# Performance work log

Hardware: AMD Instinct MI355X
Metric: run time of the kernel (lower is better)

The kernel has to match this reference:

```python
import jax, jax.numpy as jnp
import numpy as np

TWO_THIRDS = 2.0 / 3.0
SEVENTEEN_SIXTHS = 17.0 / 6.0


def _grid():
    # torch: cat(-flip(logspace(-2,2,100)**2), [0], logspace(-2,2,100)**2) -> 201 points
    gp = jnp.logspace(-2.0, 2.0, 100, dtype=jnp.float32) ** 2
    return jnp.concatenate([-gp[::-1], jnp.zeros((1,), jnp.float32), gp])


def _trapz_w(x):
    # trapezoidal quadrature weights so that trapz(f, x) == sum(f * w)
    dx = jnp.diff(x)
    w = jnp.zeros_like(x)
    return w.at[:-1].add(0.5 * dx).at[1:].add(0.5 * dx)


def setup_inputs() -> dict:
    key = jax.random.key(0)
    k1k, kyk, kzk = jax.random.split(key, 3)
    k1 = jnp.sort(jax.random.uniform(k1k, (512,), jnp.float32, 0.01, 1.0))  # positive wavenumbers
    dy = jax.random.uniform(kyk, (64,), jnp.float32, 0.0, 50.0)  # spanwise separations [m]
    dz = jax.random.uniform(kzk, (64,), jnp.float32, 0.0, 50.0)  # vertical separations [m]
    return {
        "k1_input": k1,
        "Delta_y": dy,
        "Delta_z": dz,
        "logLengthScale": jnp.float32(np.log(0.7 * 42.0)),
        "logTimeScale": jnp.float32(np.log(3.9)),
        "logMagnitude": jnp.float32(0.0),
    }


def reference(k1_input, Delta_y, Delta_z, logLengthScale, logTimeScale, logMagnitude):
    L = jnp.exp(logLengthScale)
    T = jnpp = jnp.exp(logTimeScale)
    M = jnp.exp(logMagnitude)
    k2g = _grid()  # [201]
    k3g = _grid()  # [201]
    # broadcasted meshgrid (never materialize a 4D stacked k tensor)
    k1 = k1_input[:, None, None]   # [Nk1,1,1]
    k2 = k2g[None, :, None]        # [1,201,1]
    k3 = k3g[None, None, :]        # [1,1,201]
    kk = k1 * k1 + k2 * k2 + k3 * k3
    # EddyLifetime 'TwoThird': beta = T * (L*|k|)^{-2/3}
    beta = T * (L * jnp.sqrt(kk)) ** (-TWO_THIRDS)
    k30 = k3 + beta * k1
    kk0 = k1 * k1 + k2 * k2 + k30 * k30
    k0L = L * jnp.sqrt(kk0)
    # von Karman energy spectrum at distorted wavevector
    E0 = M * k0L ** 4 / (1.0 + k0L * k0L) ** SEVENTEEN_SIXTHS
    # RDT spectral tensor, 11-component (module uses Phi[0] for Phi11, Phi33 and Phi13)
    s = k1 * k1 + k2 * k2
    C1 = beta * k1 * k1 * (kk0 - 2.0 * k30 * k30 + beta * k1 * k30) / (kk * s)
    C2 = k2 * kk0 / s ** 1.5 * jnp.arctan2(beta * k1 * jnp.sqrt(s), kk0 - k30 * k1 * beta)
    zeta1 = C1 - (k2 / k1) * C2
    Phi11 = E0 / (4.0 * jnp.pi * kk0 * kk0) * (
        kk0 - k1 * k1 - 2.0 * k1 * k30 * zeta1 + s * zeta1 * zeta1
    )  # [Nk1,201,201]
    # double trapezoid over (k2,k3) as weighted sums
    w2 = _trapz_w(k2g)
    w3 = _trapz_w(k3g)
    F1 = jnp.einsum('aij,i,j->a', Phi11, w2, w3)  # = F3
    den = jnp.sqrt(F1 * F1)
    # exp(i(k2*dy + k3*dz)) is separable -> factor the nested loop into two einsums
    Pw = (Phi11 * w2[None, :, None] * w3[None, None, :]).astype(jnp.complex64)
    E3 = jnp.exp(1j * k3g[:, None] * Delta_z[None, :])  # [201,Nz]
    E2 = jnp.exp(1j * k2g[:, None] * Delta_y[None, :])  # [201,Ny]
    A = jnp.einsum('aij,jz->aiz', Pw, E3)   # [Nk1,201,Nz]
    I = jnp.einsum('aiz,iy->ayz', A, E2)    # [Nk1,Ny,Nz]
    return jnp.real(I) / den[:, None, None]
```

## Files before the change

kernel.cpp:

```cpp
#include <hip/hip_runtime.h>
#include <math.h>

#define BLOCK 256
#define LOG2_10 3.3219280948873623f
#define PI_F 3.14159265358979f
#define INV2PI 0.15915494309189535f
#define PW_SCALE 256.0f

#define SP 128
#define SA 128
#define ST 64

typedef _Float16 half8 __attribute__((ext_vector_type(8)));
typedef _Float16 half4 __attribute__((ext_vector_type(4)));
typedef _Float16 half2v __attribute__((ext_vector_type(2)));
typedef float f32x4 __attribute__((ext_vector_type(4)));

__device__ __forceinline__ float fast_cos(float x_rev) {
    return __builtin_amdgcn_cosf(__builtin_amdgcn_fractf(x_rev));
}

__device__ __forceinline__ float atan2_pos(float y, float x) {
    float ax = __builtin_fabsf(x);
    float mn = fminf(ax, y), mx = fmaxf(ax, y);
    float a = mn * __builtin_amdgcn_rcpf(mx);
    float t = a * a;
    float p = fmaf(fmaf(fmaf(fmaf(fmaf(-0.0117212f, t, 0.05265332f), t,
              -0.11643287f), t, 0.19354346f), t, -0.33262347f), t, 0.99997726f);
    p *= a;
    p = (y > ax) ? (1.57079632679f - p) : p;
    p = (x < 0.0f) ? (3.14159265359f - p) : p;
    return p;
}

__global__ __launch_bounds__(BLOCK, 2)
void spectral_kernel(const float* __restrict__ k1_in,
                     const float* __restrict__ dy_in,
                     const float* __restrict__ dz_in,
                     const float* __restrict__ plogL,
                     const float* __restrict__ plogT,
                     const float* __restrict__ plogM,
                     float* __restrict__ out)
{
    __shared__ __attribute__((aligned(16))) _Float16 s_phiT[32 * SP];
    __shared__ __attribute__((aligned(16))) _Float16 s_B3T[64 * SP];
    __shared__ __attribute__((aligned(16))) _Float16 s_A2[64 * SA];
    __shared__ __attribute__((aligned(16))) _Float16 s_TcT[64 * ST];
    __shared__ float  s_grid[204];
    __shared__ float2 s_gw[204];
    __shared__ float  s_dy[64], s_dz[64];
    __shared__ float  s_red[8];

    const int t    = threadIdx.x;
    const int a    = blockIdx.x;
    const int lane = t & 63;
    const int w    = t >> 6;
    const int n16  = lane & 15;
    const int quad = lane >> 4;

    const float L  = expf(plogL[0]);
    const float Tt = expf(plogT[0]);
    const float M  = expf(plogM[0]);
    const float L2 = L * L;
    const float k1   = k1_in[a];
    const float k1sq = k1 * k1;
    const float rk1  = __builtin_amdgcn_rcpf(k1);
    const float cM0  = (M * 0.25f / PI_F) * PW_SCALE;

    if (t < 204) {
        int tt = min(t, 200);
        float v;
        if (tt < 100)       v = -exp2f(LOG2_10 * (-4.0f + 8.0f * (float)(99 - tt) * (1.0f/99.0f)));
        else if (tt == 100) v = 0.0f;
        else                v =  exp2f(LOG2_10 * (-4.0f + 8.0f * (float)(tt - 101) * (1.0f/99.0f)));
        s_grid[t] = v;
    }
    if (t < 64) { s_dy[t] = dy_in[t]; s_dz[t] = dz_in[t]; }
    __syncthreads();

    if (t < 204) {
        float wv = 0.0f;
        if (t == 0)          wv = 0.5f * (s_grid[1] - s_grid[0]);
        else if (t < 200)    wv = 0.5f * (s_grid[t+1] - s_grid[t-1]);
        else if (t == 200)   wv = 0.5f * (s_grid[200] - s_grid[199]);
        s_gw[t] = make_float2(s_grid[t], wv);
    }
    {
        const int jjp = lane;
        const int jj0 = 2 * jjp, jj1 = jj0 + 1;
        const float g0 = s_grid[min(100 + jj0, 203)];
        const float g1 = s_grid[min(100 + jj1, 203)];
        const int jjg  = jjp >> 2;
        for (int m = 0; m < 16; ++m) {
            int z = w + 4 * m;
            float dzr = s_dz[z] * INV2PI;
            float c0 = (jj0 <= 100) ? fast_cos(g0 * dzr) : 0.0f;
            float c1 = (jj1 <= 100) ? fast_cos(g1 * dzr) : 0.0f;
            half2v pr; pr.x = (_Float16)c0; pr.y = (_Float16)c1;
            *(half2v*)&s_B3T[z * SP + ((jjg ^ (z & 7)) << 3) + (jj0 & 7)] = pr;
        }
    }
    {
        float dyr = s_dy[lane] * INV2PI;
        for (int k = 0; k < 16; ++k) {
            int iip = w + 4 * k;
            int i0 = 2 * iip, i1 = i0 + 1;
            float c0 = (i0 <= 100) ? fast_cos(s_grid[min(100 + i0, 203)] * dyr) : 0.0f;
            float c1 = (i1 <= 100) ? fast_cos(s_grid[min(100 + i1, 203)] * dyr) : 0.0f;
            half2v pr; pr.x = (_Float16)c0; pr.y = (_Float16)c1;
            int off = lane * SA + (((iip >> 2) ^ (lane & 7)) << 3) + ((iip & 3) << 1);
            *(half2v*)&s_A2[off] = pr;
        }
    }
    {
        half8 zz = {};
        *(half8*)&s_phiT[t * 8] = zz;
        *(half8*)&s_phiT[(t + 256) * 8] = zz;
    }
    __syncthreads();

    float f1 = 0.0f;
    f32x4 acc2[4];
    #pragma unroll
    for (int i = 0; i < 4; ++i) acc2[i] = (f32x4){0.f, 0.f, 0.f, 0.f};

    const int il = t >> 3;
    const int jb = t & 7;

    for (int c = 0; c < 4; ++c) {
        if (c < 3) {
            const int ii = c * 32 + il;
            const float k2  = s_gw[100 + ii].x;
            const float w2m = s_gw[100 + ii].y * ((ii == 0) ? 1.0f : 2.0f);
            const float cM  = cM0 * w2m;
            const float s   = k1sq + k2 * k2;
            const float rs  = __builtin_amdgcn_rsqf(s);
            const float sqs = s * rs;
            const float s15inv = rs * rs * rs;
            const float k2ok1  = k2 * rk1;

            #pragma unroll 2
            for (int k = 0; k < 13; ++k) {
                const int jj = jb + (k << 3);
                const bool act = (jj <= 100);
                const float2 gwv = s_gw[100 + (act ? jj : 0)];
                const float g = gwv.x, w3 = gwv.y;
                const float kk   = fmaf(g, g, s);
                const float beta = Tt * __builtin_amdgcn_exp2f((-1.0f/3.0f) * __builtin_amdgcn_logf(L2 * kk));
                const float bk1  = beta * k1;
                const float rkks = __builtin_amdgcn_rcpf(kk * s);
                const float bkk1 = bk1 * k1;
                float k30a = bk1 - g,        k30b = bk1 + g;
                float k3sa = k30a * k30a,    k3sb = k30b * k30b;
                float kk0a = s + k3sa,       kk0b = s + k3sb;
                float ua   = L2 * kk0a,      ub   = L2 * kk0b;
                float e0a  = ua * ua * __builtin_amdgcn_exp2f((-17.0f/6.0f) * __builtin_amdgcn_logf(1.0f + ua));
                float e0b  = ub * ub * __builtin_amdgcn_exp2f((-17.0f/6.0f) * __builtin_amdgcn_logf(1.0f + ub));
                float C1a  = bkk1 * (s - k3sa + bk1 * k30a) * rkks;
                float C1b  = bkk1 * (s - k3sb + bk1 * k30b) * rkks;
                float tha  = atan2_pos(bk1 * sqs, kk0a - k30a * bk1);
                float thb  = atan2_pos(bk1 * sqs, kk0b - k30b * bk1);
                float za   = C1a - k2ok1 * (k2 * kk0a * s15inv * tha);
                float zb   = C1b - k2ok1 * (k2 * kk0b * s15inv * thb);
                float rka  = __builtin_amdgcn_rcpf(kk0a);
                float rkb  = __builtin_amdgcn_rcpf(kk0b);
                float qqa  = fmaf(fmaf(s, za, -2.0f * k1 * k30a), za, kk0a - k1sq);
                float qqb  = fmaf(fmaf(s, zb, -2.0f * k1 * k30b), zb, kk0b - k1sq);
                float pws  = fmaf(e0a * qqa, rka * rka, e0b * qqb * rkb * rkb);
                float scale = (jj == 0) ? 0.5f : 1.0f;
                float val = act ? (pws * cM * w3 * scale) : 0.0f;
                f1 += val;
                s_phiT[il * SP + (((jj >> 3) ^ (il & 7)) << 3) + (jj & 7)] = (_Float16)val;
            }
        } else {
            for (int idx = t; idx < 432; idx += 256) {
                half8 zz = {};
                *(half8*)&s_phiT[5 * SP + idx * 8] = zz;
            }
            #pragma unroll
            for (int m = 0; m < 2; ++m) {
                const int widx = t + 256 * m;
                if (widx < 505) {
                    const int il3 = widx / 101;
                    const int jj  = widx - il3 * 101;
                    const int ii  = 96 + il3;
                    const float k2  = s_gw[100 + ii].x;
                    const float cM  = cM0 * (s_gw[100 + ii].y * 2.0f);
                    const float s   = k1sq + k2 * k2;
                    const float rs  = __builtin_amdgcn_rsqf(s);
                    const float sqs = s * rs;
                    const float s15inv = rs * rs * rs;
                    const float k2ok1  = k2 * rk1;
                    const float2 gwv = s_gw[100 + jj];
                    const float g = gwv.x, w3 = gwv.y;
                    const float kk   = fmaf(g, g, s);
                    const float beta = Tt * __builtin_amdgcn_exp2f((-1.0f/3.0f) * __builtin_amdgcn_logf(L2 * kk));
                    const float bk1  = beta * k1;
                    const float rkks = __builtin_amdgcn_rcpf(kk * s);
                    const float bkk1 = bk1 * k1;
                    float k30a = bk1 - g,        k30b = bk1 + g;
                    float k3sa = k30a * k30a,    k3sb = k30b * k30b;
                    float kk0a = s + k3sa,       kk0b = s + k3sb;
                    float ua   = L2 * kk0a,      ub   = L2 * kk0b;
                    float e0a  = ua * ua * __builtin_amdgcn_exp2f((-17.0f/6.0f) * __builtin_amdgcn_logf(1.0f + ua));
                    float e0b  = ub * ub * __builtin_amdgcn_exp2f((-17.0f/6.0f) * __builtin_amdgcn_logf(1.0f + ub));
                    float C1a  = bkk1 * (s - k3sa + bk1 * k30a) * rkks;
                    float C1b  = bkk1 * (s - k3sb + bk1 * k30b) * rkks;
                    float tha  = atan2_pos(bk1 * sqs, kk0a - k30a * bk1);
                    float thb  = atan2_pos(bk1 * sqs, kk0b - k30b * bk1);
                    float za   = C1a - k2ok1 * (k2 * kk0a * s15inv * tha);
                    float zb   = C1b - k2ok1 * (k2 * kk0b * s15inv * thb);
                    float rka  = __builtin_amdgcn_rcpf(kk0a);
                    float rkb  = __builtin_amdgcn_rcpf(kk0b);
                    float qqa  = fmaf(fmaf(s, za, -2.0f * k1 * k30a), za, kk0a - k1sq);
                    float qqb  = fmaf(fmaf(s, zb, -2.0f * k1 * k30b), zb, kk0b - k1sq);
                    float pws  = fmaf(e0a * qqa, rka * rka, e0b * qqb * rkb * rkb);
                    float scale = (jj == 0) ? 0.5f : 1.0f;
                    float val = pws * cM * w3 * scale;
                    f1 += val;
                    s_phiT[il3 * SP + (((jj >> 3) ^ (il3 & 7)) << 3) + (jj & 7)] = (_Float16)val;
                }
            }
        }
        __syncthreads();

        {
            const int mt  = w & 1;
            const int nt0 = (w >> 1) << 1;
            f32x4 acc1a = {0.f,0.f,0.f,0.f}, acc1b = {0.f,0.f,0.f,0.f};
            const int arow  = mt * 16 + n16;
            const int brow0 = nt0 * 16 + n16;
            const int brow1 = brow0 + 16;
            #pragma unroll
            for (int ks = 0; ks < 4; ++ks) {
                int kg = ks * 4 + quad;
                half8 af  = *(const half8*)&s_phiT[arow  * SP + ((kg ^ (arow  & 7)) << 3)];
                half8 bf0 = *(const half8*)&s_B3T [brow0 * SP + ((kg ^ (brow0 & 7)) << 3)];
                half8 bf1 = *(const half8*)&s_B3T [brow1 * SP + ((kg ^ (brow1 & 7)) << 3)];
                acc1a = __builtin_amdgcn_mfma_f32_16x16x32_f16(af, bf0, acc1a, 0, 0, 0);
                acc1b = __builtin_amdgcn_mfma_f32_16x16x32_f16(af, bf1, acc1b, 0, 0, 0);
            }
            const int ii0 = mt * 16 + quad * 4;
            const int g   = ii0 >> 3;
            const int wi  = ii0 & 7;
            {
                int z = brow0;
                half4 hv; hv.x=(_Float16)acc1a.x; hv.y=(_Float16)acc1a.y;
                hv.z=(_Float16)acc1a.z; hv.w=(_Float16)acc1a.w;
                *(half4*)&s_TcT[z * ST + ((g ^ (z & 7)) << 3) + wi] = hv;
            }
            {
                int z = brow1;
                half4 hv; hv.x=(_Float16)acc1b.x; hv.y=(_Float16)acc1b.y;
                hv.z=(_Float16)acc1b.z; hv.w=(_Float16)acc1b.w;
                *(half4*)&s_TcT[z * ST + ((g ^ (z & 7)) << 3) + wi] = hv;
            }
        }
        __syncthreads();

        {
            const int yrow = w * 16 + n16;
            const int G = c * 4 + quad;
            half8 a2f = *(const half8*)&s_A2[yrow * SA + ((G ^ (yrow & 7)) << 3)];
            #pragma unroll
            for (int nt = 0; nt < 4; ++nt) {
                int z = nt * 16 + n16;
                half8 bf = *(const half8*)&s_TcT[z * ST + ((quad ^ (z & 7)) << 3)];
                acc2[nt] = __builtin_amdgcn_mfma_f32_16x16x32_f16(a2f, bf, acc2[nt], 0, 0, 0);
            }
        }
        __syncthreads();
    }

    float v = f1;
    #pragma unroll
    for (int off = 32; off > 0; off >>= 1) v += __shfl_down(v, off, 64);
    if (lane == 0) s_red[w] = v;
    __syncthreads();
    if (t == 0) s_red[4] = 1.0f / fabsf(s_red[0] + s_red[1] + s_red[2] + s_red[3]);
    __syncthreads();
    const float rden = s_red[4];

    float* op = out + ((size_t)a << 12);
    #pragma unroll
    for (int nt = 0; nt < 4; ++nt) {
        int z = nt * 16 + n16;
        #pragma unroll
        for (int r = 0; r < 4; ++r) {
            int y = w * 16 + quad * 4 + r;
            op[y * 64 + z] = acc2[nt][r] * rden;
        }
    }
}

extern "C" void kernel_launch(void* const* d_in, const int* in_sizes, int n_in,
                              void* d_out, int out_size, void* d_ws, size_t ws_size,
                              hipStream_t stream) {
    const float* k1 = (const float*)d_in[0];
    const float* dy = (const float*)d_in[1];
    const float* dz = (const float*)d_in[2];
    const float* lL = (const float*)d_in[3];
    const float* lT = (const float*)d_in[4];
    const float* lM = (const float*)d_in[5];
    float* outp = (float*)d_out;
    hipLaunchKernelGGL(spectral_kernel, dim3(512), dim3(BLOCK), 0, stream,
                       k1, dy, dz, lL, lT, lM, outp);
}
```

Measured before the change: 88.62 us.

## Double block size to 512 threads and simplify spectrum algebra

Raises the workgroup from 4 to 8 wavefronts and redistributes the Phi evaluation, the cosine table fills and both MFMA stages so each wave handles half as many tiles. The von Karman factor is rewritten so that k0L^4/kk0^2 collapses to a constant L^4, removing two reciprocals and several multiplies per pair. The aim is more latency hiding for the transcendental-heavy spectral evaluation, at the cost of tighter register limits under the new launch bounds and more barrier participants.

```diff
diff --git a/kernel.cpp b/kernel.cpp
--- a/kernel.cpp
+++ b/kernel.cpp
@@ -1,7 +1,7 @@
 #include <hip/hip_runtime.h>
 #include <math.h>
 
-#define BLOCK 256
+#define BLOCK 512
 #define LOG2_10 3.3219280948873623f
 #define PI_F 3.14159265358979f
 #define INV2PI 0.15915494309189535f
@@ -33,7 +33,33 @@
     return p;
 }
 
-__global__ __launch_bounds__(BLOCK, 2)
+__device__ __forceinline__ float phi_pair(float k1, float k1sq, float Tt, float L2,
+                                          float s, float sqs, float s15inv,
+                                          float k2, float k2ok1, float g) {
+    const float kk   = fmaf(g, g, s);
+    const float beta = Tt * __builtin_amdgcn_exp2f((-1.0f/3.0f) * __builtin_amdgcn_logf(L2 * kk));
+    const float bk1  = beta * k1;
+    const float rkks = __builtin_amdgcn_rcpf(kk * s);
+    const float bkk1 = bk1 * k1;
+    const float yv   = bk1 * sqs;
+    float k30a = bk1 - g,      k30b = bk1 + g;
+    float k3sa = k30a * k30a,  k3sb = k30b * k30b;
+    float kk0a = s + k3sa,     kk0b = s + k3sb;
+    float ua   = L2 * kk0a,    ub   = L2 * kk0b;
+    float pa = __builtin_amdgcn_exp2f((-17.0f/6.0f) * __builtin_amdgcn_logf(1.0f + ua));
+    float pb = __builtin_amdgcn_exp2f((-17.0f/6.0f) * __builtin_amdgcn_logf(1.0f + ub));
+    float C1a = bkk1 * (s - k3sa + bk1 * k30a) * rkks;
+    float C1b = bkk1 * (s - k3sb + bk1 * k30b) * rkks;
+    float tha = atan2_pos(yv, kk0a - k30a * bk1);
+    float thb = atan2_pos(yv, kk0b - k30b * bk1);
+    float za  = C1a - k2ok1 * (k2 * kk0a * s15inv * tha);
+    float zb  = C1b - k2ok1 * (k2 * kk0b * s15inv * thb);
+    float qqa = fmaf(fmaf(s, za, -2.0f * k1 * k30a), za, kk0a - k1sq);
+    float qqb = fmaf(fmaf(s, zb, -2.0f * k1 * k30b), zb, kk0b - k1sq);
+    return fmaf(pa, qqa, pb * qqb);
+}
+
+__global__ __launch_bounds__(BLOCK, 4)
 void spectral_kernel(const float* __restrict__ k1_in,
                      const float* __restrict__ dy_in,
                      const float* __restrict__ dz_in,
@@ -49,7 +75,7 @@
     __shared__ float  s_grid[204];
     __shared__ float2 s_gw[204];
     __shared__ float  s_dy[64], s_dz[64];
-    __shared__ float  s_red[8];
+    __shared__ float  s_red[16];
 
     const int t    = threadIdx.x;
     const int a    = blockIdx.x;
@@ -62,10 +88,11 @@
     const float Tt = expf(plogT[0]);
     const float M  = expf(plogM[0]);
     const float L2 = L * L;
+    const float L4 = L2 * L2;
     const float k1   = k1_in[a];
     const float k1sq = k1 * k1;
     const float rk1  = __builtin_amdgcn_rcpf(k1);
-    const float cM0  = (M * 0.25f / PI_F) * PW_SCALE;
+    const float cM0  = (M * 0.25f / PI_F) * PW_SCALE * L4;
 
     if (t < 204) {
         int tt = min(t, 200);
@@ -86,13 +113,15 @@
         s_gw[t] = make_float2(s_grid[t], wv);
     }
     {
-        const int jjp = lane;
+        const int jjp = t & 63;
+        const int zg  = t >> 6;
         const int jj0 = 2 * jjp, jj1 = jj0 + 1;
         const float g0 = s_grid[min(100 + jj0, 203)];
         const float g1 = s_grid[min(100 + jj1, 203)];
         const int jjg  = jjp >> 2;
-        for (int m = 0; m < 16; ++m) {
-            int z = w + 4 * m;
+        #pragma unroll
+        for (int m = 0; m < 8; ++m) {
+            int z = zg + 8 * m;
             float dzr = s_dz[z] * INV2PI;
             float c0 = (jj0 <= 100) ? fast_cos(g0 * dzr) : 0.0f;
             float c1 = (jj1 <= 100) ? fast_cos(g1 * dzr) : 0.0f;
@@ -101,31 +130,35 @@
         }
     }
     {
-        float dyr = s_dy[lane] * INV2PI;
-        for (int k = 0; k < 16; ++k) {
-            int iip = w + 4 * k;
-            int i0 = 2 * iip, i1 = i0 + 1;
-            float c0 = (i0 <= 100) ? fast_cos(s_grid[min(100 + i0, 203)] * dyr) : 0.0f;
-            float c1 = (i1 <= 100) ? fast_cos(s_grid[min(100 + i1, 203)] * dyr) : 0.0f;
+        const int iip = t & 63;
+        const int yg  = t >> 6;
+        const int i0 = 2 * iip, i1 = i0 + 1;
+        const float g0 = s_grid[min(100 + i0, 203)];
+        const float g1 = s_grid[min(100 + i1, 203)];
+        #pragma unroll
+        for (int m = 0; m < 8; ++m) {
+            int y = yg + 8 * m;
+            float dyr = s_dy[y] * INV2PI;
+            float c0 = (i0 <= 100) ? fast_cos(g0 * dyr) : 0.0f;
+            float c1 = (i1 <= 100) ? fast_cos(g1 * dyr) : 0.0f;
             half2v pr; pr.x = (_Float16)c0; pr.y = (_Float16)c1;
-            int off = lane * SA + (((iip >> 2) ^ (lane & 7)) << 3) + ((iip & 3) << 1);
+            int off = y * SA + (((iip >> 2) ^ (y & 7)) << 3) + ((iip & 3) << 1);
             *(half2v*)&s_A2[off] = pr;
         }
     }
     {
         half8 zz = {};
         *(half8*)&s_phiT[t * 8] = zz;
-        *(half8*)&s_phiT[(t + 256) * 8] = zz;
     }
     __syncthreads();
 
     float f1 = 0.0f;
-    f32x4 acc2[4];
-    #pragma unroll
-    for (int i = 0; i < 4; ++i) acc2[i] = (f32x4){0.f, 0.f, 0.f, 0.f};
-
-    const int il = t >> 3;
-    const int jb = t & 7;
+    f32x4 acc2[2];
+    acc2[0] = (f32x4){0.f, 0.f, 0.f, 0.f};
+    acc2[1] = (f32x4){0.f, 0.f, 0.f, 0.f};
+
+    const int il = t >> 4;
+    const int jb = t & 15;
 
     for (int c = 0; c < 4; ++c) {
         if (c < 3) {
@@ -140,133 +173,76 @@
             const float k2ok1  = k2 * rk1;
 
             #pragma unroll 2
-            for (int k = 0; k < 13; ++k) {
-                const int jj = jb + (k << 3);
+            for (int k = 0; k < 7; ++k) {
+                const int jj = jb + (k << 4);
                 const bool act = (jj <= 100);
                 const float2 gwv = s_gw[100 + (act ? jj : 0)];
                 const float g = gwv.x, w3 = gwv.y;
-                const float kk   = fmaf(g, g, s);
-                const float beta = Tt * __builtin_amdgcn_exp2f((-1.0f/3.0f) * __builtin_amdgcn_logf(L2 * kk));
-                const float bk1  = beta * k1;
-                const float rkks = __builtin_amdgcn_rcpf(kk * s);
-                const float bkk1 = bk1 * k1;
-                float k30a = bk1 - g,        k30b = bk1 + g;
-                float k3sa = k30a * k30a,    k3sb = k30b * k30b;
-                float kk0a = s + k3sa,       kk0b = s + k3sb;
-                float ua   = L2 * kk0a,      ub   = L2 * kk0b;
-                float e0a  = ua * ua * __builtin_amdgcn_exp2f((-17.0f/6.0f) * __builtin_amdgcn_logf(1.0f + ua));
-                float e0b  = ub * ub * __builtin_amdgcn_exp2f((-17.0f/6.0f) * __builtin_amdgcn_logf(1.0f + ub));
-                float C1a  = bkk1 * (s - k3sa + bk1 * k30a) * rkks;
-                float C1b  = bkk1 * (s - k3sb + bk1 * k30b) * rkks;
-                float tha  = atan2_pos(bk1 * sqs, kk0a - k30a * bk1);
-                float thb  = atan2_pos(bk1 * sqs, kk0b - k30b * bk1);
-                float za   = C1a - k2ok1 * (k2 * kk0a * s15inv * tha);
-                float zb   = C1b - k2ok1 * (k2 * kk0b * s15inv * thb);
-                float rka  = __builtin_amdgcn_rcpf(kk0a);
-                float rkb  = __builtin_amdgcn_rcpf(kk0b);
-                float qqa  = fmaf(fmaf(s, za, -2.0f * k1 * k30a), za, kk0a - k1sq);
-                float qqb  = fmaf(fmaf(s, zb, -2.0f * k1 * k30b), zb, kk0b - k1sq);
-                float pws  = fmaf(e0a * qqa, rka * rka, e0b * qqb * rkb * rkb);
+                float pws = phi_pair(k1, k1sq, Tt, L2, s, sqs, s15inv, k2, k2ok1, g);
                 float scale = (jj == 0) ? 0.5f : 1.0f;
                 float val = act ? (pws * cM * w3 * scale) : 0.0f;
                 f1 += val;
                 s_phiT[il * SP + (((jj >> 3) ^ (il & 7)) << 3) + (jj & 7)] = (_Float16)val;
             }
         } else {
-            for (int idx = t; idx < 432; idx += 256) {
+            if (t < 432) {
                 half8 zz = {};
-                *(half8*)&s_phiT[5 * SP + idx * 8] = zz;
-            }
-            #pragma unroll
-            for (int m = 0; m < 2; ++m) {
-                const int widx = t + 256 * m;
-                if (widx < 505) {
-                    const int il3 = widx / 101;
-                    const int jj  = widx - il3 * 101;
-                    const int ii  = 96 + il3;
-                    const float k2  = s_gw[100 + ii].x;
-                    const float cM  = cM0 * (s_gw[100 + ii].y * 2.0f);
-                    const float s   = k1sq + k2 * k2;
-                    const float rs  = __builtin_amdgcn_rsqf(s);
-                    const float sqs = s * rs;
-                    const float s15inv = rs * rs * rs;
-                    const float k2ok1  = k2 * rk1;
-                    const float2 gwv = s_gw[100 + jj];
-                    const float g = gwv.x, w3 = gwv.y;
-                    const float kk   = fmaf(g, g, s);
-                    const float beta = Tt * __builtin_amdgcn_exp2f((-1.0f/3.0f) * __builtin_amdgcn_logf(L2 * kk));
-                    const float bk1  = beta * k1;
-                    const float rkks = __builtin_amdgcn_rcpf(kk * s);
-                    const float bkk1 = bk1 * k1;
-                    float k30a = bk1 - g,        k30b = bk1 + g;
-                    float k3sa = k30a * k30a,    k3sb = k30b * k30b;
-                    float kk0a = s + k3sa,       kk0b = s + k3sb;
-                    float ua   = L2 * kk0a,      ub   = L2 * kk0b;
-                    float e0a  = ua * ua * __builtin_amdgcn_exp2f((-17.0f/6.0f) * __builtin_amdgcn_logf(1.0f + ua));
-                    float e0b  = ub * ub * __builtin_amdgcn_exp2f((-17.0f/6.0f) * __builtin_amdgcn_logf(1.0f + ub));
-                    float C1a  = bkk1 * (s - k3sa + bk1 * k30a) * rkks;
-                    float C1b  = bkk1 * (s - k3sb + bk1 * k30b) * rkks;
-                    float tha  = atan2_pos(bk1 * sqs, kk0a - k30a * bk1);
-                    float thb  = atan2_pos(bk1 * sqs, kk0b - k30b * bk1);
-                    float za   = C1a - k2ok1 * (k2 * kk0a * s15inv * tha);
-                    float zb   = C1b - k2ok1 * (k2 * kk0b * s15inv * thb);
-                    float rka  = __builtin_amdgcn_rcpf(kk0a);
-                    float rkb  = __builtin_amdgcn_rcpf(kk0b);
-                    float qqa  = fmaf(fmaf(s, za, -2.0f * k1 * k30a), za, kk0a - k1sq);
-                    float qqb  = fmaf(fmaf(s, zb, -2.0f * k1 * k30b), zb, kk0b - k1sq);
-                    float pws  = fmaf(e0a * qqa, rka * rka, e0b * qqb * rkb * rkb);
-                    float scale = (jj == 0) ? 0.5f : 1.0f;
-                    float val = pws * cM * w3 * scale;
-                    f1 += val;
-                    s_phiT[il3 * SP + (((jj >> 3) ^ (il3 & 7)) << 3) + (jj & 7)] = (_Float16)val;
-                }
+                *(half8*)&s_phiT[5 * SP + t * 8] = zz;
+            }
+            if (t < 505) {
+                const int il3 = t / 101;
+                const int jj  = t - il3 * 101;
+                const int ii  = 96 + il3;
+                const float k2  = s_gw[100 + ii].x;
+                const float cM  = cM0 * (s_gw[100 + ii].y * 2.0f);
+                const float s   = k1sq + k2 * k2;
+                const float rs  = __builtin_amdgcn_rsqf(s);
+                const float sqs = s * rs;
+                const float s15inv = rs * rs * rs;
+                const float k2ok1  = k2 * rk1;
+                const float2 gwv = s_gw[100 + jj];
+                float pws = phi_pair(k1, k1sq, Tt, L2, s, sqs, s15inv, k2, k2ok1, gwv.x);
+                float scale = (jj == 0) ? 0.5f : 1.0f;
+                float val = pws * cM * gwv.y * scale;
+                f1 += val;
+                s_phiT[il3 * SP + (((jj >> 3) ^ (il3 & 7)) << 3) + (jj & 7)] = (_Float16)val;
             }
         }
         __syncthreads();
 
         {
-            const int mt  = w & 1;
-            const int nt0 = (w >> 1) << 1;
-            f32x4 acc1a = {0.f,0.f,0.f,0.f}, acc1b = {0.f,0.f,0.f,0.f};
-            const int arow  = mt * 16 + n16;
-            const int brow0 = nt0 * 16 + n16;
-            const int brow1 = brow0 + 16;
+            const int mt = w & 1;
+            const int nt = w >> 1;
+            f32x4 acc1 = {0.f, 0.f, 0.f, 0.f};
+            const int arow = mt * 16 + n16;
+            const int brow = nt * 16 + n16;
             #pragma unroll
             for (int ks = 0; ks < 4; ++ks) {
                 int kg = ks * 4 + quad;
-                half8 af  = *(const half8*)&s_phiT[arow  * SP + ((kg ^ (arow  & 7)) << 3)];
-                half8 bf0 = *(const half8*)&s_B3T [brow0 * SP + ((kg ^ (brow0 & 7)) << 3)];
-                half8 bf1 = *(const half8*)&s_B3T [brow1 * SP + ((kg ^ (brow1 & 7)) << 3)];
-                acc1a = __builtin_amdgcn_mfma_f32_16x16x32_f16(af, bf0, acc1a, 0, 0, 0);
-                acc1b = __builtin_amdgcn_mfma_f32_16x16x32_f16(af, bf1, acc1b, 0, 0, 0);
+                half8 af = *(const half8*)&s_phiT[arow * SP + ((kg ^ (arow & 7)) << 3)];
+                half8 bf = *(const half8*)&s_B3T [brow * SP + ((kg ^ (brow & 7)) << 3)];
+                acc1 = __builtin_amdgcn_mfma_f32_16x16x32_f16(af, bf, acc1, 0, 0, 0);
             }
             const int ii0 = mt * 16 + quad * 4;
-            const int g   = ii0 >> 3;
+            const int gg  = ii0 >> 3;
             const int wi  = ii0 & 7;
-            {
-                int z = brow0;
-                half4 hv; hv.x=(_Float16)acc1a.x; hv.y=(_Float16)acc1a.y;
-                hv.z=(_Float16)acc1a.z; hv.w=(_Float16)acc1a.w;
-                *(half4*)&s_TcT[z * ST + ((g ^ (z & 7)) << 3) + wi] = hv;
-            }
-            {
-                int z = brow1;
-                half4 hv; hv.x=(_Float16)acc1b.x; hv.y=(_Float16)acc1b.y;
-                hv.z=(_Float16)acc1b.z; hv.w=(_Float16)acc1b.w;
-                *(half4*)&s_TcT[z * ST + ((g ^ (z & 7)) << 3) + wi] = hv;
-            }
+            half4 hv; hv.x=(_Float16)acc1.x; hv.y=(_Float16)acc1.y;
+            hv.z=(_Float16)acc1.z; hv.w=(_Float16)acc1.w;
+            *(half4*)&s_TcT[brow * ST + ((gg ^ (brow & 7)) << 3) + wi] = hv;
         }
         __syncthreads();
 
         {
-            const int yrow = w * 16 + n16;
+            const int yt  = w >> 1;
+            const int zt0 = (w & 1) * 2;
+            const int yrow = yt * 16 + n16;
             const int G = c * 4 + quad;
             half8 a2f = *(const half8*)&s_A2[yrow * SA + ((G ^ (yrow & 7)) << 3)];
             #pragma unroll
-            for (int nt = 0; nt < 4; ++nt) {
-                int z = nt * 16 + n16;
+            for (int p = 0; p < 2; ++p) {
+                int z = (zt0 + p) * 16 + n16;
                 half8 bf = *(const half8*)&s_TcT[z * ST + ((quad ^ (z & 7)) << 3)];
-                acc2[nt] = __builtin_amdgcn_mfma_f32_16x16x32_f16(a2f, bf, acc2[nt], 0, 0, 0);
+                acc2[p] = __builtin_amdgcn_mfma_f32_16x16x32_f16(a2f, bf, acc2[p], 0, 0, 0);
             }
         }
         __syncthreads();
@@ -277,18 +253,27 @@
     for (int off = 32; off > 0; off >>= 1) v += __shfl_down(v, off, 64);
     if (lane == 0) s_red[w] = v;
     __syncthreads();
-    if (t == 0) s_red[4] = 1.0f / fabsf(s_red[0] + s_red[1] + s_red[2] + s_red[3]);
-    __syncthreads();
-    const float rden = s_red[4];
+    if (t == 0) {
+        float sum = 0.0f;
+        #pragma unroll
+        for (int i = 0; i < 8; ++i) sum += s_red[i];
+        s_red[8] = 1.0f / fabsf(sum);
+    }
+    __syncthreads();
+    const float rden = s_red[8];
 
     float* op = out + ((size_t)a << 12);
-    #pragma unroll
-    for (int nt = 0; nt < 4; ++nt) {
-        int z = nt * 16 + n16;
-        #pragma unroll
-        for (int r = 0; r < 4; ++r) {
-            int y = w * 16 + quad * 4 + r;
-            op[y * 64 + z] = acc2[nt][r] * rden;
+    {
+        const int yt  = w >> 1;
+        const int zt0 = (w & 1) * 2;
+        #pragma unroll
+        for (int p = 0; p < 2; ++p) {
+            int z = (zt0 + p) * 16 + n16;
+            #pragma unroll
+            for (int r = 0; r < 4; ++r) {
+                int y = yt * 16 + quad * 4 + r;
+                op[y * 64 + z] = acc2[p][r] * rden;
+            }
         }
     }
 }
```

New measurement: 87.80 us. Within noise of the previous version (-0.9%).

## Split Phi evaluation into separate wide kernel writing fp16 image to workspace

Applied to the files above, without the earlier changes.

Moves the transcendental-heavy Phi11 evaluation out of the per-k1 MFMA kernel into a new phi_kernel that runs 2048 blocks (four chunks per k1) and writes swizzled fp16 tiles to workspace. The spectral kernel then loads these tiles from global memory, reduces F1 from the fp16 values, and runs only the two-stage MFMA contraction, with launch bounds raised for occupancy. Phi math is also algebraically simplified (folding L^4 into the constant and removing reciprocals of kk0) and the last chunk is remapped for better lane utilization. The cost is an extra launch plus a global round trip for the intermediate, and F1 now sums fp16-rounded values, which changes precision slightly.

```diff
diff --git a/kernel.cpp b/kernel.cpp
--- a/kernel.cpp
+++ b/kernel.cpp
@@ -1,7 +1,6 @@
 #include <hip/hip_runtime.h>
 #include <math.h>
 
-#define BLOCK 256
 #define LOG2_10 3.3219280948873623f
 #define PI_F 3.14159265358979f
 #define INV2PI 0.15915494309189535f
@@ -33,13 +32,141 @@
     return p;
 }
 
-__global__ __launch_bounds__(BLOCK, 2)
-void spectral_kernel(const float* __restrict__ k1_in,
-                     const float* __restrict__ dy_in,
+__device__ __forceinline__ float phi_pair(float k1, float k1sq, float n2k1, float Tt, float L2,
+                                          float s, float sqs, float k2sc, float g) {
+    const float kk   = fmaf(g, g, s);
+    const float beta = Tt * __builtin_amdgcn_exp2f((-1.0f/3.0f) * __builtin_amdgcn_logf(L2 * kk));
+    const float bk1  = beta * k1;
+    const float Qh   = bk1 * g;
+    const float xa   = kk - Qh, xb = kk + Qh;
+    const float sg   = 2.0f * s - kk;
+    const float cc   = (bk1 * k1) * __builtin_amdgcn_rcpf(kk * s);
+    const float C1a  = cc * (sg + Qh), C1b = cc * (sg - Qh);
+    const float yv   = bk1 * sqs;
+    const float tha  = atan2_pos(yv, xa);
+    const float thb  = atan2_pos(yv, xb);
+    const float R    = fmaf(bk1, bk1, kk);
+    const float kk0a = fmaf(-2.0f, Qh, R), kk0b = fmaf(2.0f, Qh, R);
+    const float ua   = L2 * kk0a, ub = L2 * kk0b;
+    const float pa = __builtin_amdgcn_exp2f((-17.0f/6.0f) * __builtin_amdgcn_logf(1.0f + ua));
+    const float pb = __builtin_amdgcn_exp2f((-17.0f/6.0f) * __builtin_amdgcn_logf(1.0f + ub));
+    const float za = C1a - k2sc * (kk0a * tha);
+    const float zb = C1b - k2sc * (kk0b * thb);
+    const float k30a = bk1 - g, k30b = bk1 + g;
+    const float qqa = fmaf(fmaf(s, za, n2k1 * k30a), za, kk0a - k1sq);
+    const float qqb = fmaf(fmaf(s, zb, n2k1 * k30b), zb, kk0b - k1sq);
+    return fmaf(pa, qqa, pb * qqb);
+}
+
+__global__ __launch_bounds__(256, 4)
+void phi_kernel(const float* __restrict__ k1_in,
+                const float* __restrict__ plogL,
+                const float* __restrict__ plogT,
+                const float* __restrict__ plogM,
+                _Float16* __restrict__ img)
+{
+    __shared__ float  s_grid[204];
+    __shared__ float2 s_gw[204];
+
+    const int t = threadIdx.x;
+    const int b = blockIdx.x;
+    const int a = b >> 2;
+    const int c = b & 3;
+
+    const float L  = expf(plogL[0]);
+    const float Tt = expf(plogT[0]);
+    const float M  = expf(plogM[0]);
+    const float L2 = L * L;
+    const float L4 = L2 * L2;
+    const float k1   = k1_in[a];
+    const float k1sq = k1 * k1;
+    const float n2k1 = -2.0f * k1;
+    const float rk1  = __builtin_amdgcn_rcpf(k1);
+    const float cM0  = (M * 0.25f / PI_F) * PW_SCALE * L4;
+
+    if (t < 204) {
+        int tt = min(t, 200);
+        float v;
+        if (tt < 100)       v = -exp2f(LOG2_10 * (-4.0f + 8.0f * (float)(99 - tt) * (1.0f/99.0f)));
+        else if (tt == 100) v = 0.0f;
+        else                v =  exp2f(LOG2_10 * (-4.0f + 8.0f * (float)(tt - 101) * (1.0f/99.0f)));
+        s_grid[t] = v;
+    }
+    __syncthreads();
+    if (t < 204) {
+        float wv = 0.0f;
+        if (t == 0)          wv = 0.5f * (s_grid[1] - s_grid[0]);
+        else if (t < 200)    wv = 0.5f * (s_grid[t+1] - s_grid[t-1]);
+        else if (t == 200)   wv = 0.5f * (s_grid[200] - s_grid[199]);
+        s_gw[t] = make_float2(s_grid[t], wv);
+    }
+    __syncthreads();
+
+    _Float16* bimg = img + (size_t)b * 4096;
+
+    if (c < 3) {
+        const int il = t >> 3;
+        const int jb = t & 7;
+        const int ii = c * 32 + il;
+        const float k2  = s_gw[100 + ii].x;
+        const float w2m = s_gw[100 + ii].y * ((ii == 0) ? 1.0f : 2.0f);
+        const float cM  = cM0 * w2m;
+        const float s   = k1sq + k2 * k2;
+        const float rs  = __builtin_amdgcn_rsqf(s);
+        const float sqs = s * rs;
+        const float k2sc = (k2 * rk1) * k2 * (rs * rs * rs);
+
+        #pragma unroll 2
+        for (int k = 0; k < 13; ++k) {
+            const int jj = jb + (k << 3);
+            const bool act = (jj <= 100);
+            const float2 gwv = s_gw[100 + (act ? jj : 0)];
+            float pws = phi_pair(k1, k1sq, n2k1, Tt, L2, s, sqs, k2sc, gwv.x);
+            float w3s = (jj == 0) ? 0.5f * gwv.y : gwv.y;
+            float val = act ? (pws * cM * w3s) : 0.0f;
+            bimg[il * SP + (((jj >> 3) ^ (il & 7)) << 3) + (jj & 7)] = (_Float16)val;
+        }
+        #pragma unroll
+        for (int m = 0; m < 3; ++m) {
+            int jj = 104 + jb + (m << 3);
+            bimg[il * SP + (((jj >> 3) ^ (il & 7)) << 3) + (jj & 7)] = (_Float16)0.0f;
+        }
+    } else {
+        const int il = t & 7;
+        const int jb = t >> 3;
+        const int ii = 96 + il;
+        const bool rowAct = (ii <= 100);
+        const int iic = min(ii, 100);
+        const float k2  = s_gw[100 + iic].x;
+        const float cM  = cM0 * (s_gw[100 + iic].y * 2.0f);
+        const float s   = k1sq + k2 * k2;
+        const float rs  = __builtin_amdgcn_rsqf(s);
+        const float sqs = s * rs;
+        const float k2sc = (k2 * rk1) * k2 * (rs * rs * rs);
+
+        #pragma unroll
+        for (int k = 0; k < 4; ++k) {
+            const int jj = jb + (k << 5);
+            const bool act = rowAct && (jj <= 100);
+            const float2 gwv = s_gw[100 + min(jj, 100)];
+            float pws = phi_pair(k1, k1sq, n2k1, Tt, L2, s, sqs, k2sc, gwv.x);
+            float w3s = (jj == 0) ? 0.5f * gwv.y : gwv.y;
+            float val = act ? (pws * cM * w3s) : 0.0f;
+            bimg[il * SP + (((jj >> 3) ^ (il & 7)) << 3) + (jj & 7)] = (_Float16)val;
+        }
+        {
+            half8 zz = {};
+            int base = 8 * SP;
+            *(half8*)&bimg[base + t * 8] = zz;
+            if (t < 128) *(half8*)&bimg[base + (t + 256) * 8] = zz;
+        }
+    }
+}
+
+__global__ __launch_bounds__(256, 3)
+void spectral_kernel(const float* __restrict__ dy_in,
                      const float* __restrict__ dz_in,
-                     const float* __restrict__ plogL,
-                     const float* __restrict__ plogT,
-                     const float* __restrict__ plogM,
+                     const _Float16* __restrict__ img,
                      float* __restrict__ out)
 {
     __shared__ __attribute__((aligned(16))) _Float16 s_phiT[32 * SP];
@@ -47,7 +174,6 @@
     __shared__ __attribute__((aligned(16))) _Float16 s_A2[64 * SA];
     __shared__ __attribute__((aligned(16))) _Float16 s_TcT[64 * ST];
     __shared__ float  s_grid[204];
-    __shared__ float2 s_gw[204];
     __shared__ float  s_dy[64], s_dz[64];
     __shared__ float  s_red[8];
 
@@ -57,15 +183,6 @@
     const int w    = t >> 6;
     const int n16  = lane & 15;
     const int quad = lane >> 4;
-
-    const float L  = expf(plogL[0]);
-    const float Tt = expf(plogT[0]);
-    const float M  = expf(plogM[0]);
-    const float L2 = L * L;
-    const float k1   = k1_in[a];
-    const float k1sq = k1 * k1;
-    const float rk1  = __builtin_amdgcn_rcpf(k1);
-    const float cM0  = (M * 0.25f / PI_F) * PW_SCALE;
 
     if (t < 204) {
         int tt = min(t, 200);
@@ -78,13 +195,6 @@
     if (t < 64) { s_dy[t] = dy_in[t]; s_dz[t] = dz_in[t]; }
     __syncthreads();
 
-    if (t < 204) {
-        float wv = 0.0f;
-        if (t == 0)          wv = 0.5f * (s_grid[1] - s_grid[0]);
-        else if (t < 200)    wv = 0.5f * (s_grid[t+1] - s_grid[t-1]);
-        else if (t == 200)   wv = 0.5f * (s_grid[200] - s_grid[199]);
-        s_gw[t] = make_float2(s_grid[t], wv);
-    }
     {
         const int jjp = lane;
         const int jj0 = 2 * jjp, jj1 = jj0 + 1;
@@ -112,11 +222,6 @@
             *(half2v*)&s_A2[off] = pr;
         }
     }
-    {
-        half8 zz = {};
-        *(half8*)&s_phiT[t * 8] = zz;
-        *(half8*)&s_phiT[(t + 256) * 8] = zz;
-    }
     __syncthreads();
 
     float f1 = 0.0f;
@@ -124,103 +229,17 @@
     #pragma unroll
     for (int i = 0; i < 4; ++i) acc2[i] = (f32x4){0.f, 0.f, 0.f, 0.f};
 
-    const int il = t >> 3;
-    const int jb = t & 7;
-
     for (int c = 0; c < 4; ++c) {
-        if (c < 3) {
-            const int ii = c * 32 + il;
-            const float k2  = s_gw[100 + ii].x;
-            const float w2m = s_gw[100 + ii].y * ((ii == 0) ? 1.0f : 2.0f);
-            const float cM  = cM0 * w2m;
-            const float s   = k1sq + k2 * k2;
-            const float rs  = __builtin_amdgcn_rsqf(s);
-            const float sqs = s * rs;
-            const float s15inv = rs * rs * rs;
-            const float k2ok1  = k2 * rk1;
-
-            #pragma unroll 2
-            for (int k = 0; k < 13; ++k) {
-                const int jj = jb + (k << 3);
-                const bool act = (jj <= 100);
-                const float2 gwv = s_gw[100 + (act ? jj : 0)];
-                const float g = gwv.x, w3 = gwv.y;
-                const float kk   = fmaf(g, g, s);
-                const float beta = Tt * __builtin_amdgcn_exp2f((-1.0f/3.0f) * __builtin_amdgcn_logf(L2 * kk));
-                const float bk1  = beta * k1;
-                const float rkks = __builtin_amdgcn_rcpf(kk * s);
-                const float bkk1 = bk1 * k1;
-                float k30a = bk1 - g,        k30b = bk1 + g;
-                float k3sa = k30a * k30a,    k3sb = k30b * k30b;
-                float kk0a = s + k3sa,       kk0b = s + k3sb;
-                float ua   = L2 * kk0a,      ub   = L2 * kk0b;
-                float e0a  = ua * ua * __builtin_amdgcn_exp2f((-17.0f/6.0f) * __builtin_amdgcn_logf(1.0f + ua));
-                float e0b  = ub * ub * __builtin_amdgcn_exp2f((-17.0f/6.0f) * __builtin_amdgcn_logf(1.0f + ub));
-                float C1a  = bkk1 * (s - k3sa + bk1 * k30a) * rkks;
-                float C1b  = bkk1 * (s - k3sb + bk1 * k30b) * rkks;
-                float tha  = atan2_pos(bk1 * sqs, kk0a - k30a * bk1);
-                float thb  = atan2_pos(bk1 * sqs, kk0b - k30b * bk1);
-                float za   = C1a - k2ok1 * (k2 * kk0a * s15inv * tha);
-                float zb   = C1b - k2ok1 * (k2 * kk0b * s15inv * thb);
-                float rka  = __builtin_amdgcn_rcpf(kk0a);
-                float rkb  = __builtin_amdgcn_rcpf(kk0b);
-                float qqa  = fmaf(fmaf(s, za, -2.0f * k1 * k30a), za, kk0a - k1sq);
-                float qqb  = fmaf(fmaf(s, zb, -2.0f * k1 * k30b), zb, kk0b - k1sq);
-                float pws  = fmaf(e0a * qqa, rka * rka, e0b * qqb * rkb * rkb);
-                float scale = (jj == 0) ? 0.5f : 1.0f;
-                float val = act ? (pws * cM * w3 * scale) : 0.0f;
-                f1 += val;
-                s_phiT[il * SP + (((jj >> 3) ^ (il & 7)) << 3) + (jj & 7)] = (_Float16)val;
-            }
-        } else {
-            for (int idx = t; idx < 432; idx += 256) {
-                half8 zz = {};
-                *(half8*)&s_phiT[5 * SP + idx * 8] = zz;
-            }
+        {
+            const _Float16* src = img + ((size_t)(a * 4 + c) << 12);
+            half8 v0 = *(const half8*)&src[t * 16];
+            half8 v1 = *(const half8*)&src[t * 16 + 8];
+            float sacc = 0.0f;
             #pragma unroll
-            for (int m = 0; m < 2; ++m) {
-                const int widx = t + 256 * m;
-                if (widx < 505) {
-                    const int il3 = widx / 101;
-                    const int jj  = widx - il3 * 101;
-                    const int ii  = 96 + il3;
-                    const float k2  = s_gw[100 + ii].x;
-                    const float cM  = cM0 * (s_gw[100 + ii].y * 2.0f);
-                    const float s   = k1sq + k2 * k2;
-                    const float rs  = __builtin_amdgcn_rsqf(s);
-                    const float sqs = s * rs;
-                    const float s15inv = rs * rs * rs;
-                    const float k2ok1  = k2 * rk1;
-                    const float2 gwv = s_gw[100 + jj];
-                    const float g = gwv.x, w3 = gwv.y;
-                    const float kk   = fmaf(g, g, s);
-                    const float beta = Tt * __builtin_amdgcn_exp2f((-1.0f/3.0f) * __builtin_amdgcn_logf(L2 * kk));
-                    const float bk1  = beta * k1;
-                    const float rkks = __builtin_amdgcn_rcpf(kk * s);
-                    const float bkk1 = bk1 * k1;
-                    float k30a = bk1 - g,        k30b = bk1 + g;
-                    float k3sa = k30a * k30a,    k3sb = k30b * k30b;
-                    float kk0a = s + k3sa,       kk0b = s + k3sb;
-                    float ua   = L2 * kk0a,      ub   = L2 * kk0b;
-                    float e0a  = ua * ua * __builtin_amdgcn_exp2f((-17.0f/6.0f) * __builtin_amdgcn_logf(1.0f + ua));
-                    float e0b  = ub * ub * __builtin_amdgcn_exp2f((-17.0f/6.0f) * __builtin_amdgcn_logf(1.0f + ub));
-                    float C1a  = bkk1 * (s - k3sa + bk1 * k30a) * rkks;
-                    float C1b  = bkk1 * (s - k3sb + bk1 * k30b) * rkks;
-                    float tha  = atan2_pos(bk1 * sqs, kk0a - k30a * bk1);
-                    float thb  = atan2_pos(bk1 * sqs, kk0b - k30b * bk1);
-                    float za   = C1a - k2ok1 * (k2 * kk0a * s15inv * tha);
-                    float zb   = C1b - k2ok1 * (k2 * kk0b * s15inv * thb);
-                    float rka  = __builtin_amdgcn_rcpf(kk0a);
-                    float rkb  = __builtin_amdgcn_rcpf(kk0b);
-                    float qqa  = fmaf(fmaf(s, za, -2.0f * k1 * k30a), za, kk0a - k1sq);
-                    float qqb  = fmaf(fmaf(s, zb, -2.0f * k1 * k30b), zb, kk0b - k1sq);
-                    float pws  = fmaf(e0a * qqa, rka * rka, e0b * qqb * rkb * rkb);
-                    float scale = (jj == 0) ? 0.5f : 1.0f;
-                    float val = pws * cM * w3 * scale;
-                    f1 += val;
-                    s_phiT[il3 * SP + (((jj >> 3) ^ (il3 & 7)) << 3) + (jj & 7)] = (_Float16)val;
-                }
-            }
+            for (int e = 0; e < 8; ++e) sacc += (float)v0[e] + (float)v1[e];
+            f1 += sacc;
+            *(half8*)&s_phiT[t * 16]     = v0;
+            *(half8*)&s_phiT[t * 16 + 8] = v1;
         }
         __syncthreads();
 
@@ -241,19 +260,19 @@
                 acc1b = __builtin_amdgcn_mfma_f32_16x16x32_f16(af, bf1, acc1b, 0, 0, 0);
             }
             const int ii0 = mt * 16 + quad * 4;
-            const int g   = ii0 >> 3;
+            const int gg  = ii0 >> 3;
             const int wi  = ii0 & 7;
             {
                 int z = brow0;
                 half4 hv; hv.x=(_Float16)acc1a.x; hv.y=(_Float16)acc1a.y;
                 hv.z=(_Float16)acc1a.z; hv.w=(_Float16)acc1a.w;
-                *(half4*)&s_TcT[z * ST + ((g ^ (z & 7)) << 3) + wi] = hv;
+                *(half4*)&s_TcT[z * ST + ((gg ^ (z & 7)) << 3) + wi] = hv;
             }
             {
                 int z = brow1;
                 half4 hv; hv.x=(_Float16)acc1b.x; hv.y=(_Float16)acc1b.y;
                 hv.z=(_Float16)acc1b.z; hv.w=(_Float16)acc1b.w;
-                *(half4*)&s_TcT[z * ST + ((g ^ (z & 7)) << 3) + wi] = hv;
+                *(half4*)&s_TcT[z * ST + ((gg ^ (z & 7)) << 3) + wi] = hv;
             }
         }
         __syncthreads();
@@ -303,6 +322,10 @@
     const float* lT = (const float*)d_in[4];
     const float* lM = (const float*)d_in[5];
     float* outp = (float*)d_out;
-    hipLaunchKernelGGL(spectral_kernel, dim3(512), dim3(BLOCK), 0, stream,
-                       k1, dy, dz, lL, lT, lM, outp);
-}
+    _Float16* img = (_Float16*)d_ws;
+
+    hipLaunchKernelGGL(phi_kernel, dim3(2048), dim3(256), 0, stream,
+                       k1, lL, lT, lM, img);
+    hipLaunchKernelGGL(spectral_kernel, dim3(512), dim3(256), 0, stream,
+                       dy, dz, img, outp);
+}
```

Measured after the change: 97.22 us. +9.7%, slower.
